# Kernel optimization log

Hardware: AMD Instinct MI355X
Metric: run time of the kernel (lower is better)

Reference implementation:

```python
import jax, jax.numpy as jnp
import numpy as np

B, C, W, H = 4, 256, 64, 64
AC = C // 4  # attn channels


def setup_inputs() -> dict:
    key = jax.random.key(0)
    ks = jax.random.split(key, 4)
    x = jax.random.normal(ks[0], (B, C, W, H), dtype=jnp.float32)
    Wq = jax.random.normal(ks[1], (AC, C), dtype=jnp.float32) * (1.0 / np.sqrt(C))
    Wk = jax.random.normal(ks[2], (AC, C), dtype=jnp.float32) * (1.0 / np.sqrt(C))
    Wv = jax.random.normal(ks[3], (C, C), dtype=jnp.float32) * (1.0 / np.sqrt(C))
    bq = jnp.zeros((AC,), dtype=jnp.float32)
    bk = jnp.zeros((AC,), dtype=jnp.float32)
    bv = jnp.zeros((C,), dtype=jnp.float32)
    gamma = jnp.zeros((1,), dtype=jnp.float32)
    return {"x": x, "Wq": Wq, "bq": bq, "Wk": Wk, "bk": bk, "Wv": Wv, "bv": bv, "gamma": gamma}


def reference(x, Wq, bq, Wk, bk, Wv, bv, gamma):
    b, c, w, h = x.shape
    n = w * h
    xf = x.reshape(b, c, n)  # [B, C, N]
    # 1x1 convs == channel GEMMs
    q = jnp.einsum('oc,bcn->bon', Wq, xf) + bq[None, :, None]  # [B, AC, N]
    k = jnp.einsum('oc,bcn->bon', Wk, xf) + bk[None, :, None]  # [B, AC, N]
    v = jnp.einsum('oc,bcn->bon', Wv, xf) + bv[None, :, None]  # [B, C, N]
    # attn[b, i, j] = sum_c q[b, c, i] * k[b, c, j]  (query transposed)
    attn = jnp.einsum('bci,bcj->bij', q, k)  # [B, N, N]
    # NOTE: non-standard softmax over dim=1 (over query index i for each column j)
    attn = jax.nn.softmax(attn, axis=1)
    # attn_out = attn @ value.T  -> [B, N, C]
    attn_out = jnp.einsum('bij,bcj->bic', attn, v)
    attn_out = attn_out.reshape(b, w, h, c).transpose(0, 3, 1, 2)  # [B, C, W, H]
    return gamma[0] * attn_out + x
```

## Files before the change

kernel.cpp:

```cpp
#include <hip/hip_runtime.h>
#include <hip/hip_bf16.h>

#define BB 4
#define CC 256
#define NN 4096
#define AC2 64
#define PP 76
#define JT 32

typedef __attribute__((ext_vector_type(4))) float f32x4;
typedef __attribute__((ext_vector_type(8))) short bf16x8;

__device__ __forceinline__ short f2bf(float f) {
    unsigned u = __builtin_bit_cast(unsigned, f);
    u = u + 0x7FFFu + ((u >> 16) & 1u);
    return (short)(u >> 16);
}
__device__ __forceinline__ float bf2f(unsigned short h) {
    unsigned u = ((unsigned)h) << 16;
    return __builtin_bit_cast(float, u);
}

__global__ __launch_bounds__(256) void prep_kernel(
    const float* __restrict__ Wq, const float* __restrict__ Wk,
    const float* __restrict__ Wv, short* __restrict__ Wb)
{
    const int idx = (blockIdx.x * 256 + threadIdx.x) * 4;
    const int o = idx >> 8, c = idx & 255;
    const float* row = (o < 64) ? (Wq + o * CC)
                     : (o < 128) ? (Wk + (o - 64) * CC)
                                 : (Wv + (o - 128) * CC);
    float4 v = *(const float4*)&row[c];
    short4 s4;
    s4.x = f2bf(v.x); s4.y = f2bf(v.y); s4.z = f2bf(v.z); s4.w = f2bf(v.w);
    *(short4*)&Wb[idx] = s4;
}

__global__ __launch_bounds__(512) void qkv_kernel(
    const float* __restrict__ x, const short* __restrict__ Wb,
    const float* __restrict__ bq, const float* __restrict__ bk,
    const float* __restrict__ bv,
    short* __restrict__ Qt, short* __restrict__ Kt, short* __restrict__ V)
{
    __shared__ __align__(16) short Xl[32 * 72];
    const int bid0 = blockIdx.x;
    const int bid = ((bid0 & 7) << 6) | (bid0 >> 3);
    const int b = bid >> 7;
    const int n0 = (bid & 127) << 5;
    const int tid = threadIdx.x;
    const int lane = tid & 63, w = tid >> 6;
    const int l15 = lane & 15, lh = lane >> 4;

    f32x4 acc[3][2];
#pragma unroll
    for (int i = 0; i < 3; ++i)
#pragma unroll
        for (int j = 0; j < 2; ++j) acc[i][j] = (f32x4){0.f, 0.f, 0.f, 0.f};

    for (int ck = 0; ck < 4; ++ck) {
        const int c0 = ck << 6;
        bf16x8 Af[3][2];
#pragma unroll
        for (int of = 0; of < 3; ++of)
#pragma unroll
            for (int ks = 0; ks < 2; ++ks)
                Af[of][ks] = *(const bf16x8*)&Wb[(size_t)(w * 48 + of * 16 + l15) * CC +
                                                 c0 + ks * 32 + (lh << 3)];
        {
            const int cr = tid >> 3, q4 = tid & 7;
            float4 v = *(const float4*)&x[((size_t)(b * CC + c0 + cr)) * NN + n0 + q4 * 4];
            Xl[(q4 * 4 + 0) * 72 + cr] = f2bf(v.x);
            Xl[(q4 * 4 + 1) * 72 + cr] = f2bf(v.y);
            Xl[(q4 * 4 + 2) * 72 + cr] = f2bf(v.z);
            Xl[(q4 * 4 + 3) * 72 + cr] = f2bf(v.w);
        }
        __syncthreads();
#pragma unroll
        for (int ks = 0; ks < 2; ++ks) {
            const int co = ks * 32 + (lh << 3);
            bf16x8 Bf[2];
#pragma unroll
            for (int nf = 0; nf < 2; ++nf)
                Bf[nf] = *(const bf16x8*)&Xl[(nf * 16 + l15) * 72 + co];
#pragma unroll
            for (int of = 0; of < 3; ++of)
#pragma unroll
                for (int nf = 0; nf < 2; ++nf)
                    acc[of][nf] = __builtin_amdgcn_mfma_f32_16x16x32_bf16(
                        Af[of][ks], Bf[nf], acc[of][nf], 0, 0, 0);
        }
        __syncthreads();
    }
#pragma unroll
    for (int of = 0; of < 3; ++of) {
        const int obase = w * 48 + of * 16 + (lh << 2);
        float bias[4];
#pragma unroll
        for (int r = 0; r < 4; ++r) {
            int o = obase + r;
            bias[r] = (o < 64) ? bq[o] : (o < 128) ? bk[o - 64] : bv[o - 128];
        }
#pragma unroll
        for (int nf = 0; nf < 2; ++nf) {
            const int n = n0 + nf * 16 + l15;
            if (obase < 128) {
                short4 pk;
                pk.x = f2bf(acc[of][nf][0] + bias[0]);
                pk.y = f2bf(acc[of][nf][1] + bias[1]);
                pk.z = f2bf(acc[of][nf][2] + bias[2]);
                pk.w = f2bf(acc[of][nf][3] + bias[3]);
                short* dst = (obase < 64)
                    ? (Qt + ((size_t)b * NN + n) * AC2 + obase)
                    : (Kt + ((size_t)b * NN + n) * AC2 + (obase - 64));
                *(short4*)dst = pk;
            } else {
#pragma unroll
                for (int r = 0; r < 4; ++r) {
                    int o = obase + r - 128;
                    V[(((size_t)b * CC + o) * NN) + n] = f2bf(acc[of][nf][r] + bias[r]);
                }
            }
        }
    }
}

__global__ __launch_bounds__(256) void stats_kernel(
    const short* __restrict__ Qt, const short* __restrict__ Kt,
    float* __restrict__ tArr)
{
    const int bid0 = blockIdx.x;
    const int bid = ((bid0 & 7) << 7) | (bid0 >> 3);
    const int b = bid >> 8;
    const int j0 = (bid & 255) << 4;
    const int tid = threadIdx.x;
    const int lane = tid & 63, w = tid >> 6;
    const int l15 = lane & 15, lh = lane >> 4;
    const short* Qb = Qt + (size_t)b * NN * AC2;

    bf16x8 Bf[2];
#pragma unroll
    for (int ks = 0; ks < 2; ++ks)
        Bf[ks] = *(const bf16x8*)&Kt[((size_t)b * NN + j0 + l15) * AC2 +
                                     ks * 32 + (lh << 3)];

    bf16x8 A0[4], A1[4];
#pragma unroll
    for (int f = 0; f < 4; ++f) {
        const size_t rowA = (size_t)(w * 1024 + f * 16 + l15);
        A0[f] = *(const bf16x8*)&Qb[rowA * AC2 + (lh << 3)];
        A1[f] = *(const bf16x8*)&Qb[rowA * AC2 + 32 + (lh << 3)];
    }

    float m_run = -INFINITY, l_run = 0.f;
    for (int ii = 0; ii < 16; ++ii) {
        bf16x8 A0n[4], A1n[4];
        const int in0 = w * 1024 + ((ii + 1) & 15) * 64;
#pragma unroll
        for (int f = 0; f < 4; ++f) {
            const size_t rowA = (size_t)(in0 + f * 16 + l15);
            A0n[f] = *(const bf16x8*)&Qb[rowA * AC2 + (lh << 3)];
            A1n[f] = *(const bf16x8*)&Qb[rowA * AC2 + 32 + (lh << 3)];
        }
        f32x4 s[4];
#pragma unroll
        for (int f = 0; f < 4; ++f) {
            f32x4 t = (f32x4){0.f, 0.f, 0.f, 0.f};
            t = __builtin_amdgcn_mfma_f32_16x16x32_bf16(A0[f], Bf[0], t, 0, 0, 0);
            t = __builtin_amdgcn_mfma_f32_16x16x32_bf16(A1[f], Bf[1], t, 0, 0, 0);
            s[f] = t;
        }
        float mx = s[0][0];
#pragma unroll
        for (int f = 0; f < 4; ++f)
#pragma unroll
            for (int r = 0; r < 4; ++r) mx = fmaxf(mx, s[f][r]);
        const float m_new = fmaxf(m_run, mx);
        float add = 0.f;
#pragma unroll
        for (int f = 0; f < 4; ++f)
#pragma unroll
            for (int r = 0; r < 4; ++r) add += __expf(s[f][r] - m_new);
        l_run = l_run * __expf(m_run - m_new) + add;
        m_run = m_new;
#pragma unroll
        for (int f = 0; f < 4; ++f) { A0[f] = A0n[f]; A1[f] = A1n[f]; }
    }
#pragma unroll
    for (int off = 16; off <= 32; off <<= 1) {
        float m2 = __shfl_xor(m_run, off);
        float l2 = __shfl_xor(l_run, off);
        float mm = fmaxf(m_run, m2);
        l_run = l_run * __expf(m_run - mm) + l2 * __expf(m2 - mm);
        m_run = mm;
    }
    __shared__ float sm[4][16];
    __shared__ float sl[4][16];
    if (lane < 16) { sm[w][lane] = m_run; sl[w][lane] = l_run; }
    __syncthreads();
    if (tid < 16) {
        float m = sm[0][tid], l = sl[0][tid];
#pragma unroll
        for (int q = 1; q < 4; ++q) {
            float m2 = sm[q][tid], l2 = sl[q][tid];
            float mm = fmaxf(m, m2);
            l = l * __expf(m - mm) + l2 * __expf(m2 - mm);
            m = mm;
        }
        tArr[(size_t)b * NN + j0 + tid] = m + __logf(l);
    }
}

__global__ __launch_bounds__(256, 4) void out_kernel(
    const short* __restrict__ Qt, const short* __restrict__ Kt,
    const short* __restrict__ V,
    const float* __restrict__ tArr,
    float* __restrict__ out)
{
    __shared__ __align__(16) short Kl[2][64 * PP];
    __shared__ __align__(16) short Pl[2][64 * PP];
    __shared__ float Tl[2][64];
    const int bid0 = blockIdx.x;
    const int bid = ((bid0 & 7) << 7) | (bid0 >> 3);
    const int jh = bid & 1;
    const int cs = (bid >> 1) & 1;
    const int itile = (bid >> 2) & 63;
    const int b = bid >> 8;
    const int i0 = itile << 6, c0 = cs << 7;
    const int jbase = jh << 11;
    const int tid = threadIdx.x;
    const int lane = tid & 63, w = tid >> 6;
    const int l15 = lane & 15, lh = lane >> 4;
    const int iw = i0 + (w << 4);

    const short* Ktb = Kt + (size_t)b * NN * AC2;
    const float* tb  = tArr + (size_t)b * NN + jbase;
    const short* Vb  = V + ((size_t)(b * CC + c0 + (w << 5))) * NN + jbase;

    const int krow = tid >> 2, kch = (tid & 3) << 4;
    const short* Ksrc = Ktb + ((size_t)(jbase + krow)) * AC2 + kch;
    short* const KlwA = &Kl[0][krow * PP + kch];
    short* const KlwB = &Kl[1][krow * PP + kch];

    bf16x8 Aq[2];
#pragma unroll
    for (int ks = 0; ks < 2; ++ks)
        Aq[ks] = *(const bf16x8*)&Qt[((size_t)b * NN + iw + l15) * AC2 +
                                     ks * 32 + (lh << 3)];

    f32x4 acc[4][2];
#pragma unroll
    for (int f = 0; f < 4; ++f)
#pragma unroll
        for (int cf = 0; cf < 2; ++cf) acc[f][cf] = (f32x4){0.f, 0.f, 0.f, 0.f};

    {
        bf16x8 k0a = *(const bf16x8*)(Ksrc + 0);
        bf16x8 k0b = *(const bf16x8*)(Ksrc + 8);
        float   t0 = (tid < 64) ? tb[tid] : 0.f;
        *(bf16x8*)(KlwA + 0) = k0a;
        *(bf16x8*)(KlwA + 8) = k0b;
        if (tid < 64) Tl[0][tid] = t0;
    }
    bf16x8 KpA = *(const bf16x8*)(Ksrc + (1 << 12));
    bf16x8 KpB = *(const bf16x8*)(Ksrc + (1 << 12) + 8);
    float  tp  = (tid < 64) ? tb[64 + tid] : 0.f;
    bf16x8 Vc[2][2];
#pragma unroll
    for (int cf = 0; cf < 2; ++cf)
#pragma unroll
        for (int ks = 0; ks < 2; ++ks)
            Vc[cf][ks] = *(const bf16x8*)&Vb[(size_t)(cf * 16 + l15) * NN +
                                             ks * 32 + (lh << 3)];
    asm volatile("s_waitcnt lgkmcnt(0)" ::: "memory");
    __builtin_amdgcn_s_barrier();
    asm volatile("" ::: "memory");

    for (int jt = 0; jt < JT; ++jt) {
        const int cur = jt & 1;
        {
            short* kd = cur ? KlwA : KlwB;
            *(bf16x8*)(kd + 0) = KpA;
            *(bf16x8*)(kd + 8) = KpB;
            if (tid < 64) Tl[cur ^ 1][tid] = tp;
        }
        {
            const size_t t2 = (size_t)((jt + 2) & (JT - 1)) << 12;
            KpA = *(const bf16x8*)(Ksrc + t2);
            KpB = *(const bf16x8*)(Ksrc + t2 + 8);
            tp  = (tid < 64) ? tb[(((jt + 2) & (JT - 1)) << 6) + tid] : 0.f;
        }
        bf16x8 Vn[2][2];
        {
            const int tv = ((jt + 1) & (JT - 1)) << 6;
#pragma unroll
            for (int cf = 0; cf < 2; ++cf)
#pragma unroll
                for (int ks = 0; ks < 2; ++ks)
                    Vn[cf][ks] = *(const bf16x8*)&Vb[(size_t)(cf * 16 + l15) * NN +
                                                     tv + ks * 32 + (lh << 3)];
        }
        short* Pw = &Pl[cur][0];
#pragma unroll
        for (int jf = 0; jf < 4; ++jf) {
            bf16x8 Ka = *(const bf16x8*)&Kl[cur][(jf * 16 + l15) * PP + (lh << 3)];
            bf16x8 Kb = *(const bf16x8*)&Kl[cur][(jf * 16 + l15) * PP + 32 + (lh << 3)];
            f32x4 s = (f32x4){0.f, 0.f, 0.f, 0.f};
            s = __builtin_amdgcn_mfma_f32_16x16x32_bf16(Aq[0], Ka, s, 0, 0, 0);
            s = __builtin_amdgcn_mfma_f32_16x16x32_bf16(Aq[1], Kb, s, 0, 0, 0);
            const float tj = Tl[cur][jf * 16 + l15];
#pragma unroll
            for (int r = 0; r < 4; ++r)
                Pw[(w * 16 + lh * 4 + r) * PP + jf * 16 + l15] =
                    f2bf(__expf(s[r] - tj));
        }
        asm volatile("s_waitcnt lgkmcnt(0)" ::: "memory");
        __builtin_amdgcn_s_barrier();
        asm volatile("" ::: "memory");
#pragma unroll
        for (int ks = 0; ks < 2; ++ks) {
#pragma unroll
            for (int f = 0; f < 4; ++f) {
                bf16x8 Ap = *(const bf16x8*)&Pw[(f * 16 + l15) * PP +
                                                ks * 32 + (lh << 3)];
#pragma unroll
                for (int cf = 0; cf < 2; ++cf)
                    acc[f][cf] = __builtin_amdgcn_mfma_f32_16x16x32_bf16(
                        Ap, Vc[cf][ks], acc[f][cf], 0, 0, 0);
            }
        }
#pragma unroll
        for (int cf = 0; cf < 2; ++cf) {
            Vc[cf][0] = Vn[cf][0]; Vc[cf][1] = Vn[cf][1];
        }
    }

    __syncthreads();
    float* Pfw = (float*)&Pl[0][0] + w * 1056;
    unsigned short* po = (unsigned short*)out;
#pragma unroll
    for (int pass = 0; pass < 2; ++pass) {
#pragma unroll
        for (int fh = 0; fh < 2; ++fh) {
            const int f = pass * 2 + fh;
#pragma unroll
            for (int cf = 0; cf < 2; ++cf)
#pragma unroll
                for (int r = 0; r < 4; ++r)
                    Pfw[(cf * 16 + l15) * 33 + fh * 16 + lh * 4 + r] = acc[f][cf][r];
        }
#pragma unroll
        for (int cq = 0; cq < 4; ++cq) {
            const int c = cq * 8 + (lane >> 3);
            const int iq = (lane & 7) * 4;
            const size_t gi = ((size_t)(b * CC + c0 + w * 32 + c)) * NN +
                              i0 + pass * 32 + iq;
#pragma unroll
            for (int k = 0; k < 4; ++k) {
                float v = Pfw[c * 33 + iq + k];
                po[(gi + k) * 2 + jh] = (unsigned short)f2bf(v);
            }
        }
    }
}

__global__ __launch_bounds__(256) void reduce_kernel(
    const float* __restrict__ x, const float* __restrict__ gamma,
    float* __restrict__ out)
{
    const float g = gamma[0];
    const size_t total = (size_t)BB * CC * NN / 4;
    for (size_t i = (size_t)blockIdx.x * 256 + threadIdx.x; i < total;
         i += (size_t)2048 * 256) {
        uint4 pv = ((const uint4*)out)[i];
        float4 xv = ((const float4*)x)[i];
        float4 o;
        o.x = g * (bf2f(pv.x & 0xFFFFu) + bf2f(pv.x >> 16)) + xv.x;
        o.y = g * (bf2f(pv.y & 0xFFFFu) + bf2f(pv.y >> 16)) + xv.y;
        o.z = g * (bf2f(pv.z & 0xFFFFu) + bf2f(pv.z >> 16)) + xv.z;
        o.w = g * (bf2f(pv.w & 0xFFFFu) + bf2f(pv.w >> 16)) + xv.w;
        ((float4*)out)[i] = o;
    }
}

extern "C" void kernel_launch(void* const* d_in, const int* in_sizes, int n_in,
                              void* d_out, int out_size, void* d_ws, size_t ws_size,
                              hipStream_t stream) {
    const float* x     = (const float*)d_in[0];
    const float* Wq    = (const float*)d_in[1];
    const float* bq    = (const float*)d_in[2];
    const float* Wk    = (const float*)d_in[3];
    const float* bk    = (const float*)d_in[4];
    const float* Wv    = (const float*)d_in[5];
    const float* bv    = (const float*)d_in[6];
    const float* gamma = (const float*)d_in[7];
    float* out = (float*)d_out;

    short* Qt = (short*)d_ws;
    short* Kt = Qt + (size_t)BB * NN * AC2;
    short* V  = Kt + (size_t)BB * NN * AC2;
    float* tArr = (float*)(V + (size_t)BB * CC * NN);
    short* Wb = (short*)(tArr + (size_t)BB * NN);

    prep_kernel<<<96, 256, 0, stream>>>(Wq, Wk, Wv, Wb);
    qkv_kernel<<<BB * 128, 512, 0, stream>>>(x, Wb, bq, bk, bv, Qt, Kt, V);
    stats_kernel<<<BB * 256, 256, 0, stream>>>(Qt, Kt, tArr);
    out_kernel<<<BB * 256, 256, 0, stream>>>(Qt, Kt, V, tArr, out);
    reduce_kernel<<<2048, 256, 0, stream>>>(x, gamma, out);
}
```

Before: 348.1 us.

## Remap blocks by XCD and swap MFMA operands to store output without LDS transpose

```diff
diff --git a/kernel.cpp b/kernel.cpp
--- a/kernel.cpp
+++ b/kernel.cpp
@@ -44,9 +44,9 @@
 {
     __shared__ __align__(16) short Xl[32 * 72];
     const int bid0 = blockIdx.x;
-    const int bid = ((bid0 & 7) << 6) | (bid0 >> 3);
-    const int b = bid >> 7;
-    const int n0 = (bid & 127) << 5;
+    const int xcd = bid0 & 7;
+    const int b = xcd >> 1, nh = xcd & 1;
+    const int n0 = (nh * 64 + (bid0 >> 3)) << 5;
     const int tid = threadIdx.x;
     const int lane = tid & 63, w = tid >> 6;
     const int l15 = lane & 15, lh = lane >> 4;
@@ -129,9 +129,9 @@
     float* __restrict__ tArr)
 {
     const int bid0 = blockIdx.x;
-    const int bid = ((bid0 & 7) << 7) | (bid0 >> 3);
-    const int b = bid >> 8;
-    const int j0 = (bid & 255) << 4;
+    const int xcd = bid0 & 7;
+    const int b = xcd >> 1;
+    const int j0 = (((xcd & 1) << 7) | (bid0 >> 3)) << 4;
     const int tid = threadIdx.x;
     const int lane = tid & 63, w = tid >> 6;
     const int l15 = lane & 15, lh = lane >> 4;
@@ -220,11 +220,10 @@
     __shared__ __align__(16) short Pl[2][64 * PP];
     __shared__ float Tl[2][64];
     const int bid0 = blockIdx.x;
-    const int bid = ((bid0 & 7) << 7) | (bid0 >> 3);
-    const int jh = bid & 1;
-    const int cs = (bid >> 1) & 1;
-    const int itile = (bid >> 2) & 63;
-    const int b = bid >> 8;
+    const int xcd = bid0 & 7;
+    const int b = xcd >> 1, jh = xcd & 1;
+    const int slot = bid0 >> 3;
+    const int itile = slot >> 1, cs = slot & 1;
     const int i0 = itile << 6, c0 = cs << 7;
     const int jbase = jh << 11;
     const int tid = threadIdx.x;
@@ -247,11 +246,11 @@
         Aq[ks] = *(const bf16x8*)&Qt[((size_t)b * NN + iw + l15) * AC2 +
                                      ks * 32 + (lh << 3)];
 
-    f32x4 acc[4][2];
-#pragma unroll
-    for (int f = 0; f < 4; ++f)
-#pragma unroll
-        for (int cf = 0; cf < 2; ++cf) acc[f][cf] = (f32x4){0.f, 0.f, 0.f, 0.f};
+    f32x4 acc[2][4];
+#pragma unroll
+    for (int cf = 0; cf < 2; ++cf)
+#pragma unroll
+        for (int f = 0; f < 4; ++f) acc[cf][f] = (f32x4){0.f, 0.f, 0.f, 0.f};
 
     {
         bf16x8 k0a = *(const bf16x8*)(Ksrc + 0);
@@ -320,12 +319,12 @@
         for (int ks = 0; ks < 2; ++ks) {
 #pragma unroll
             for (int f = 0; f < 4; ++f) {
-                bf16x8 Ap = *(const bf16x8*)&Pw[(f * 16 + l15) * PP +
+                bf16x8 Bp = *(const bf16x8*)&Pw[(f * 16 + l15) * PP +
                                                 ks * 32 + (lh << 3)];
 #pragma unroll
                 for (int cf = 0; cf < 2; ++cf)
-                    acc[f][cf] = __builtin_amdgcn_mfma_f32_16x16x32_bf16(
-                        Ap, Vc[cf][ks], acc[f][cf], 0, 0, 0);
+                    acc[cf][f] = __builtin_amdgcn_mfma_f32_16x16x32_bf16(
+                        Vc[cf][ks], Bp, acc[cf][f], 0, 0, 0);
             }
         }
 #pragma unroll
@@ -334,30 +333,16 @@
         }
     }
 
-    __syncthreads();
-    float* Pfw = (float*)&Pl[0][0] + w * 1056;
     unsigned short* po = (unsigned short*)out;
 #pragma unroll
-    for (int pass = 0; pass < 2; ++pass) {
-#pragma unroll
-        for (int fh = 0; fh < 2; ++fh) {
-            const int f = pass * 2 + fh;
-#pragma unroll
-            for (int cf = 0; cf < 2; ++cf)
-#pragma unroll
-                for (int r = 0; r < 4; ++r)
-                    Pfw[(cf * 16 + l15) * 33 + fh * 16 + lh * 4 + r] = acc[f][cf][r];
-        }
-#pragma unroll
-        for (int cq = 0; cq < 4; ++cq) {
-            const int c = cq * 8 + (lane >> 3);
-            const int iq = (lane & 7) * 4;
-            const size_t gi = ((size_t)(b * CC + c0 + w * 32 + c)) * NN +
-                              i0 + pass * 32 + iq;
-#pragma unroll
-            for (int k = 0; k < 4; ++k) {
-                float v = Pfw[c * 33 + iq + k];
-                po[(gi + k) * 2 + jh] = (unsigned short)f2bf(v);
+    for (int cf = 0; cf < 2; ++cf) {
+#pragma unroll
+        for (int r = 0; r < 4; ++r) {
+            const int c = c0 + (w << 5) + cf * 16 + (lh << 2) + r;
+#pragma unroll
+            for (int f = 0; f < 4; ++f) {
+                const size_t gi = ((size_t)(b * CC + c)) * NN + i0 + f * 16 + l15;
+                po[gi * 2 + jh] = (unsigned short)f2bf(acc[cf][f][r]);
             }
         }
     }
```

Measured after the change: 345.4 us. No clear change (-0.8%).
